# Performance work log

Measured on AMD Instinct MI355X. Metric: run time of the kernel, lower is better.

The kernel has to match this reference:

```python
import jax, jax.numpy as jnp
import numpy as np

B, T, I, H, O = 512, 1024, 15, 64, 11

def setup_inputs() -> dict:
    key = jax.random.key(0)
    ks = jax.random.split(key, 7)
    s_ih = 1.0 / np.sqrt(H)
    return {
        "x": jax.random.normal(ks[0], (B, T, I), dtype=jnp.float32),
        # torch nn.RNN params: weight_ih_l0 [H,I], weight_hh_l0 [H,H], biases [H]
        "W_ih": jax.random.uniform(ks[1], (H, I), jnp.float32, -s_ih, s_ih),
        "b_ih": jax.random.uniform(ks[2], (H,), jnp.float32, -s_ih, s_ih),
        "W_hh": jax.random.uniform(ks[3], (H, H), jnp.float32, -s_ih, s_ih),
        "b_hh": jax.random.uniform(ks[4], (H,), jnp.float32, -s_ih, s_ih),
        # decoder Linear(64, 11)
        "W_dec": jax.random.uniform(ks[5], (O, H), jnp.float32, -s_ih, s_ih),
        "b_dec": jax.random.uniform(ks[6], (O,), jnp.float32, -s_ih, s_ih),
    }

def reference(x, W_ih, b_ih, W_hh, b_hh, W_dec, b_dec):
    # Precompute input projection for all timesteps: [T, B, H]
    xproj = jnp.einsum("bti,hi->tbh", x, W_ih) + b_ih + b_hh
    h0 = jnp.zeros((x.shape[0], W_hh.shape[0]), dtype=x.dtype)

    def step(h, xp_t):
        h_new = jax.nn.relu(xp_t + h @ W_hh.T)  # [B, H]
        return h_new, h_new

    h_last, hs = jax.lax.scan(step, h0, xproj)  # hs: [T, B, H]
    out_seq = jnp.transpose(hs, (1, 0, 2))       # [B, T, H]
    out = jax.nn.relu(jnp.einsum("bth,oh->bto", out_seq, W_dec) + b_dec)
    h = h_last[None]  # [1, B, H] matching torch num_layers dim
    return (out, h)
```

## Files before the change

### kernel.cpp

```cpp
#include <hip/hip_runtime.h>
#include <hip/hip_fp16.h>
#include <stdint.h>

#define BB 512
#define TT 1024
#define II 15
#define HH 64
#define OO 11
#define NC (TT / 64)

typedef __fp16 half2v __attribute__((ext_vector_type(2)));
typedef _Float16 half8 __attribute__((ext_vector_type(8)));
typedef float floatx4 __attribute__((ext_vector_type(4)));
typedef int int4v __attribute__((ext_vector_type(4)));

union PK { int i; half2v h; float f; };
union AU { int4v i; half8 h; };

__device__ __forceinline__ half2v i2h2(int v) { PK u; u.i = v; return u.h; }
__device__ __forceinline__ int h22i(half2v v) { PK u; u.h = v; return u.i; }

__device__ __forceinline__ float FDOT2(half2v a, half2v b, float c) {
    return __builtin_amdgcn_fdot2(a, b, c, false);
}

__device__ __forceinline__ float lane_xor1(float v) {
    PK u; u.f = v;
    u.i = __builtin_amdgcn_mov_dpp(u.i, 0xB1, 0xF, 0xF, false);
    return u.f;
}

__device__ __forceinline__ float lane_xor2(float v) {
    PK u; u.f = v;
    u.i = __builtin_amdgcn_mov_dpp(u.i, 0x4E, 0xF, 0xF, false);
    return u.f;
}

__device__ __forceinline__ void block_sync() {
    asm volatile("s_waitcnt lgkmcnt(0)" ::: "memory");
    __builtin_amdgcn_s_barrier();
}

__global__ __launch_bounds__(256) void rnn_fused(
    const float* __restrict__ x, const float* __restrict__ W_ih,
    const float* __restrict__ b_ih, const float* __restrict__ W_hh,
    const float* __restrict__ b_hh, const float* __restrict__ W_dec,
    const float* __restrict__ b_dec, float* __restrict__ out,
    float* __restrict__ h_last)
{
    __shared__ __align__(16) int xpack[2][64 * 8];
    __shared__ __align__(16) float xsbuf[2][2][64 * 64];
    __shared__ __align__(16) _Float16 hring[2][128][HH];
    const int tid  = threadIdx.x;
    const int lane = tid & 63;
    const int wid  = tid >> 6;
    const int w = wid & 1;
    const int b = blockIdx.x * 2 + w;
    const float* xb = x + (size_t)b * TT * II;

    if (wid < 2) {
        const int nl = lane & 15;
        const int kq = lane >> 4;
        half8 bf[4][2];
#pragma unroll
        for (int g = 0; g < 4; ++g)
#pragma unroll
            for (int s = 0; s < 2; ++s)
#pragma unroll
                for (int j = 0; j < 8; ++j)
                    bf[g][s][j] = (_Float16)W_hh[(16 * g + nl) * HH +
                                                 32 * s + 8 * kq + j];

        int bpidx[8];
#pragma unroll
        for (int jj = 0; jj < 4; ++jj) {
            bpidx[jj]     = kq * 32 + 8 * jj;
            bpidx[jj + 4] = bpidx[jj] + 128;
        }
        const bool bsel4 = (lane & 16) != 0;
        const bool bsel5 = (lane & 32) != 0;
        const floatx4 zc = {0.0f, 0.0f, 0.0f, 0.0f};

        block_sync();

        float h = 0.0f;
        int hpk = 0;

        for (int c = 0; c < NC; ++c) {
            const float* xsp = &xsbuf[w][c & 1][0];
            for (int to = 0; to < 64; to += 8) {
#pragma unroll
                for (int u = 0; u < 8; ++u) {
                    const int ts = to + u;
                    const int t = c * 64 + ts;
                    const float xsv = xsp[ts * 64 + lane];

                    const int r0 = __builtin_amdgcn_ds_bpermute(bpidx[0], hpk);
                    const int r1 = __builtin_amdgcn_ds_bpermute(bpidx[1], hpk);
                    const int r2 = __builtin_amdgcn_ds_bpermute(bpidx[2], hpk);
                    const int r3 = __builtin_amdgcn_ds_bpermute(bpidx[3], hpk);
                    const int r4 = __builtin_amdgcn_ds_bpermute(bpidx[4], hpk);
                    const int r5 = __builtin_amdgcn_ds_bpermute(bpidx[5], hpk);
                    const int r6 = __builtin_amdgcn_ds_bpermute(bpidx[6], hpk);
                    const int r7 = __builtin_amdgcn_ds_bpermute(bpidx[7], hpk);
                    AU au0; au0.i = (int4v){r0, r1, r2, r3};
                    AU au1; au1.i = (int4v){r4, r5, r6, r7};
                    const half8 a0 = au0.h;
                    const half8 a1 = au1.h;

                    floatx4 c0 = __builtin_amdgcn_mfma_f32_16x16x32_f16(a0, bf[0][0], zc, 0, 0, 0);
                    floatx4 d0 = __builtin_amdgcn_mfma_f32_16x16x32_f16(a1, bf[0][1], zc, 0, 0, 0);
                    floatx4 c1 = __builtin_amdgcn_mfma_f32_16x16x32_f16(a0, bf[1][0], zc, 0, 0, 0);
                    floatx4 d1 = __builtin_amdgcn_mfma_f32_16x16x32_f16(a1, bf[1][1], zc, 0, 0, 0);
                    floatx4 c2 = __builtin_amdgcn_mfma_f32_16x16x32_f16(a0, bf[2][0], zc, 0, 0, 0);
                    floatx4 d2 = __builtin_amdgcn_mfma_f32_16x16x32_f16(a1, bf[2][1], zc, 0, 0, 0);
                    floatx4 c3 = __builtin_amdgcn_mfma_f32_16x16x32_f16(a0, bf[3][0], zc, 0, 0, 0);
                    floatx4 d3 = __builtin_amdgcn_mfma_f32_16x16x32_f16(a1, bf[3][1], zc, 0, 0, 0);

                    const float v0 = c0[0] + d0[0];
                    const float v1 = c1[0] + d1[0];
                    const float v2 = c2[0] + d2[0];
                    const float v3 = c3[0] + d3[0];
                    const float r01 = bsel4 ? v1 : v0;
                    const float r23 = bsel4 ? v3 : v2;
                    const float hpre = bsel5 ? r23 : r01;

                    h = fmaxf(hpre + xsv, 0.0f);
                    hring[w][t & 127][lane] = (_Float16)h;

                    hpk = h22i(__builtin_amdgcn_cvt_pkrtz(h, lane_xor1(h)));
                }
            }
            block_sync();
        }
        h_last[b * HH + lane] = h;
    } else {
        half2v wx[8];
#pragma unroll
        for (int j = 0; j < 7; ++j)
            wx[j] = __builtin_amdgcn_cvt_pkrtz(W_ih[lane * II + 2 * j],
                                               W_ih[lane * II + 2 * j + 1]);
        wx[7] = __builtin_amdgcn_cvt_pkrtz(W_ih[lane * II + 14],
                                           b_ih[lane] + b_hh[lane]);

        const int od = lane >> 2;
        const int oc = (od < OO) ? od : 0;
        const int ks = lane & 3;
        half2v wdec[8];
#pragma unroll
        for (int p = 0; p < 8; ++p)
            wdec[p] = __builtin_amdgcn_cvt_pkrtz(
                W_dec[oc * HH + (ks * 8 + p) * 2],
                W_dec[oc * HH + (ks * 8 + p) * 2 + 1]);
        const float bd = b_dec[oc];
        const bool dostore = (ks == 0) && (od < OO);
        float* outb = out + (size_t)b * TT * OO + od;

        auto stage_xs = [&](int chunk) __attribute__((always_inline)) {
            const float* xc = xb + (size_t)(chunk * 64 + lane) * II;
            float cf[II];
#pragma unroll
            for (int i = 0; i < II; ++i) cf[i] = xc[i];
            int4v p0, p1;
            p0.x = h22i(__builtin_amdgcn_cvt_pkrtz(cf[0], cf[1]));
            p0.y = h22i(__builtin_amdgcn_cvt_pkrtz(cf[2], cf[3]));
            p0.z = h22i(__builtin_amdgcn_cvt_pkrtz(cf[4], cf[5]));
            p0.w = h22i(__builtin_amdgcn_cvt_pkrtz(cf[6], cf[7]));
            p1.x = h22i(__builtin_amdgcn_cvt_pkrtz(cf[8], cf[9]));
            p1.y = h22i(__builtin_amdgcn_cvt_pkrtz(cf[10], cf[11]));
            p1.z = h22i(__builtin_amdgcn_cvt_pkrtz(cf[12], cf[13]));
            p1.w = h22i(__builtin_amdgcn_cvt_pkrtz(cf[14], 1.0f));
            *(int4v*)&xpack[w][lane * 8] = p0;
            *(int4v*)&xpack[w][lane * 8 + 4] = p1;

            const int4v* xp4 = (const int4v*)&xpack[w][0];
            float* xsd = &xsbuf[w][chunk & 1][0];
#pragma unroll 4
            for (int ts = 0; ts < 64; ++ts) {
                const int4v xv0 = xp4[2 * ts];
                const int4v xv1 = xp4[2 * ts + 1];
                float t0 = FDOT2(i2h2(xv0.x), wx[0], 0.0f);
                float t1 = FDOT2(i2h2(xv0.y), wx[1], 0.0f);
                float t2 = FDOT2(i2h2(xv0.z), wx[2], 0.0f);
                float t3 = FDOT2(i2h2(xv0.w), wx[3], 0.0f);
                float t4 = FDOT2(i2h2(xv1.x), wx[4], 0.0f);
                float t5 = FDOT2(i2h2(xv1.y), wx[5], 0.0f);
                float t6 = FDOT2(i2h2(xv1.z), wx[6], 0.0f);
                float t7 = FDOT2(i2h2(xv1.w), wx[7], 0.0f);
                xsd[ts * 64 + lane] = ((t0 + t1) + (t2 + t3)) +
                                      ((t4 + t5) + (t6 + t7));
            }
        };

        auto decode_chunk = [&](int c) __attribute__((always_inline)) {
#pragma unroll 4
            for (int lt = 0; lt < 64; ++lt) {
                const int t = c * 64 + lt;
                const char* row = (const char*)&hring[w][t & 127][0];
                const int4v d0 = *(const int4v*)(row + ks * 32);
                const int4v d1 = *(const int4v*)(row + ks * 32 + 16);
                float dacc = FDOT2(i2h2(d0.x), wdec[0], 0.0f);
                dacc = FDOT2(i2h2(d0.y), wdec[1], dacc);
                dacc = FDOT2(i2h2(d0.z), wdec[2], dacc);
                dacc = FDOT2(i2h2(d0.w), wdec[3], dacc);
                dacc = FDOT2(i2h2(d1.x), wdec[4], dacc);
                dacc = FDOT2(i2h2(d1.y), wdec[5], dacc);
                dacc = FDOT2(i2h2(d1.z), wdec[6], dacc);
                dacc = FDOT2(i2h2(d1.w), wdec[7], dacc);
                dacc += lane_xor1(dacc);
                dacc += lane_xor2(dacc);
                if (dostore)
                    outb[(size_t)t * OO] = fmaxf(dacc + bd, 0.0f);
            }
        };

        stage_xs(0);
        block_sync();

        for (int c = 0; c < NC; ++c) {
            if (c + 1 < NC) stage_xs(c + 1);
            if (c >= 1) decode_chunk(c - 1);
            block_sync();
        }
        decode_chunk(NC - 1);
    }
}

extern "C" void kernel_launch(void* const* d_in, const int* in_sizes, int n_in,
                              void* d_out, int out_size, void* d_ws, size_t ws_size,
                              hipStream_t stream) {
    const float* x     = (const float*)d_in[0];
    const float* W_ih  = (const float*)d_in[1];
    const float* b_ih  = (const float*)d_in[2];
    const float* W_hh  = (const float*)d_in[3];
    const float* b_hh  = (const float*)d_in[4];
    const float* W_dec = (const float*)d_in[5];
    const float* b_dec = (const float*)d_in[6];

    float* out    = (float*)d_out;
    float* h_last = out + (size_t)BB * TT * OO;

    rnn_fused<<<BB / 2, 256, 0, stream>>>(x, W_ih, b_ih, W_hh, b_hh,
                                          W_dec, b_dec, out, h_last);
}
```

Baseline: 251.3 us.

## Interleave two batch recurrences in one wave and halve block size

Each block now uses one recurrence wave that advances two independent batch rows in lockstep, issuing both rows' bpermutes before their MFMAs. A single helper wave stages the input projections and decodes outputs for both rows. The aim is to hide the latency of the serial per-step dependency chain by overlapping two chains in one wave, instead of using two mostly stalled waves. The risk is that the single helper wave, now doing double the work per chunk, becomes the bottleneck, and that the longer per-step instruction stream lengthens the critical path.

```diff
diff --git a/kernel.cpp b/kernel.cpp
--- a/kernel.cpp
+++ b/kernel.cpp
@@ -41,24 +41,23 @@
     __builtin_amdgcn_s_barrier();
 }
 
-__global__ __launch_bounds__(256) void rnn_fused(
+__global__ __launch_bounds__(128) void rnn_fused(
     const float* __restrict__ x, const float* __restrict__ W_ih,
     const float* __restrict__ b_ih, const float* __restrict__ W_hh,
     const float* __restrict__ b_hh, const float* __restrict__ W_dec,
     const float* __restrict__ b_dec, float* __restrict__ out,
     float* __restrict__ h_last)
 {
-    __shared__ __align__(16) int xpack[2][64 * 8];
+    __shared__ __align__(16) int xpack[64 * 8];
     __shared__ __align__(16) float xsbuf[2][2][64 * 64];
     __shared__ __align__(16) _Float16 hring[2][128][HH];
     const int tid  = threadIdx.x;
     const int lane = tid & 63;
     const int wid  = tid >> 6;
-    const int w = wid & 1;
-    const int b = blockIdx.x * 2 + w;
-    const float* xb = x + (size_t)b * TT * II;
-
-    if (wid < 2) {
+    const int bA = blockIdx.x * 2;
+    const int bB = bA + 1;
+
+    if (wid == 0) {
         const int nl = lane & 15;
         const int kq = lane >> 4;
         half8 bf[4][2];
@@ -83,57 +82,79 @@
 
         block_sync();
 
-        float h = 0.0f;
-        int hpk = 0;
+        float hA = 0.0f, hB = 0.0f;
+        int hpkA = 0, hpkB = 0;
 
         for (int c = 0; c < NC; ++c) {
-            const float* xsp = &xsbuf[w][c & 1][0];
+            const float* xspA = &xsbuf[0][c & 1][0];
+            const float* xspB = &xsbuf[1][c & 1][0];
             for (int to = 0; to < 64; to += 8) {
 #pragma unroll
                 for (int u = 0; u < 8; ++u) {
                     const int ts = to + u;
                     const int t = c * 64 + ts;
-                    const float xsv = xsp[ts * 64 + lane];
-
-                    const int r0 = __builtin_amdgcn_ds_bpermute(bpidx[0], hpk);
-                    const int r1 = __builtin_amdgcn_ds_bpermute(bpidx[1], hpk);
-                    const int r2 = __builtin_amdgcn_ds_bpermute(bpidx[2], hpk);
-                    const int r3 = __builtin_amdgcn_ds_bpermute(bpidx[3], hpk);
-                    const int r4 = __builtin_amdgcn_ds_bpermute(bpidx[4], hpk);
-                    const int r5 = __builtin_amdgcn_ds_bpermute(bpidx[5], hpk);
-                    const int r6 = __builtin_amdgcn_ds_bpermute(bpidx[6], hpk);
-                    const int r7 = __builtin_amdgcn_ds_bpermute(bpidx[7], hpk);
-                    AU au0; au0.i = (int4v){r0, r1, r2, r3};
-                    AU au1; au1.i = (int4v){r4, r5, r6, r7};
-                    const half8 a0 = au0.h;
-                    const half8 a1 = au1.h;
-
-                    floatx4 c0 = __builtin_amdgcn_mfma_f32_16x16x32_f16(a0, bf[0][0], zc, 0, 0, 0);
-                    floatx4 d0 = __builtin_amdgcn_mfma_f32_16x16x32_f16(a1, bf[0][1], zc, 0, 0, 0);
-                    floatx4 c1 = __builtin_amdgcn_mfma_f32_16x16x32_f16(a0, bf[1][0], zc, 0, 0, 0);
-                    floatx4 d1 = __builtin_amdgcn_mfma_f32_16x16x32_f16(a1, bf[1][1], zc, 0, 0, 0);
-                    floatx4 c2 = __builtin_amdgcn_mfma_f32_16x16x32_f16(a0, bf[2][0], zc, 0, 0, 0);
-                    floatx4 d2 = __builtin_amdgcn_mfma_f32_16x16x32_f16(a1, bf[2][1], zc, 0, 0, 0);
-                    floatx4 c3 = __builtin_amdgcn_mfma_f32_16x16x32_f16(a0, bf[3][0], zc, 0, 0, 0);
-                    floatx4 d3 = __builtin_amdgcn_mfma_f32_16x16x32_f16(a1, bf[3][1], zc, 0, 0, 0);
-
-                    const float v0 = c0[0] + d0[0];
-                    const float v1 = c1[0] + d1[0];
-                    const float v2 = c2[0] + d2[0];
-                    const float v3 = c3[0] + d3[0];
-                    const float r01 = bsel4 ? v1 : v0;
-                    const float r23 = bsel4 ? v3 : v2;
-                    const float hpre = bsel5 ? r23 : r01;
-
-                    h = fmaxf(hpre + xsv, 0.0f);
-                    hring[w][t & 127][lane] = (_Float16)h;
-
-                    hpk = h22i(__builtin_amdgcn_cvt_pkrtz(h, lane_xor1(h)));
+                    const float xsvA = xspA[ts * 64 + lane];
+                    const float xsvB = xspB[ts * 64 + lane];
+
+                    int rA[8], rB[8];
+#pragma unroll
+                    for (int j = 0; j < 8; ++j)
+                        rA[j] = __builtin_amdgcn_ds_bpermute(bpidx[j], hpkA);
+#pragma unroll
+                    for (int j = 0; j < 8; ++j)
+                        rB[j] = __builtin_amdgcn_ds_bpermute(bpidx[j], hpkB);
+                    __builtin_amdgcn_sched_barrier(0);
+
+                    {
+                        AU u0; u0.i = (int4v){rA[0], rA[1], rA[2], rA[3]};
+                        AU u1; u1.i = (int4v){rA[4], rA[5], rA[6], rA[7]};
+                        const half8 a0 = u0.h, a1 = u1.h;
+                        floatx4 c0 = __builtin_amdgcn_mfma_f32_16x16x32_f16(a0, bf[0][0], zc, 0, 0, 0);
+                        floatx4 d0 = __builtin_amdgcn_mfma_f32_16x16x32_f16(a1, bf[0][1], zc, 0, 0, 0);
+                        floatx4 c1 = __builtin_amdgcn_mfma_f32_16x16x32_f16(a0, bf[1][0], zc, 0, 0, 0);
+                        floatx4 d1 = __builtin_amdgcn_mfma_f32_16x16x32_f16(a1, bf[1][1], zc, 0, 0, 0);
+                        floatx4 c2 = __builtin_amdgcn_mfma_f32_16x16x32_f16(a0, bf[2][0], zc, 0, 0, 0);
+                        floatx4 d2 = __builtin_amdgcn_mfma_f32_16x16x32_f16(a1, bf[2][1], zc, 0, 0, 0);
+                        floatx4 c3 = __builtin_amdgcn_mfma_f32_16x16x32_f16(a0, bf[3][0], zc, 0, 0, 0);
+                        floatx4 d3 = __builtin_amdgcn_mfma_f32_16x16x32_f16(a1, bf[3][1], zc, 0, 0, 0);
+                        const float v0 = c0[0] + d0[0];
+                        const float v1 = c1[0] + d1[0];
+                        const float v2 = c2[0] + d2[0];
+                        const float v3 = c3[0] + d3[0];
+                        const float r01 = bsel4 ? v1 : v0;
+                        const float r23 = bsel4 ? v3 : v2;
+                        hA = fmaxf((bsel5 ? r23 : r01) + xsvA, 0.0f);
+                        hring[0][t & 127][lane] = (_Float16)hA;
+                        hpkA = h22i(__builtin_amdgcn_cvt_pkrtz(hA, lane_xor1(hA)));
+                    }
+                    {
+                        AU u0; u0.i = (int4v){rB[0], rB[1], rB[2], rB[3]};
+                        AU u1; u1.i = (int4v){rB[4], rB[5], rB[6], rB[7]};
+                        const half8 a0 = u0.h, a1 = u1.h;
+                        floatx4 c0 = __builtin_amdgcn_mfma_f32_16x16x32_f16(a0, bf[0][0], zc, 0, 0, 0);
+                        floatx4 d0 = __builtin_amdgcn_mfma_f32_16x16x32_f16(a1, bf[0][1], zc, 0, 0, 0);
+                        floatx4 c1 = __builtin_amdgcn_mfma_f32_16x16x32_f16(a0, bf[1][0], zc, 0, 0, 0);
+                        floatx4 d1 = __builtin_amdgcn_mfma_f32_16x16x32_f16(a1, bf[1][1], zc, 0, 0, 0);
+                        floatx4 c2 = __builtin_amdgcn_mfma_f32_16x16x32_f16(a0, bf[2][0], zc, 0, 0, 0);
+                        floatx4 d2 = __builtin_amdgcn_mfma_f32_16x16x32_f16(a1, bf[2][1], zc, 0, 0, 0);
+                        floatx4 c3 = __builtin_amdgcn_mfma_f32_16x16x32_f16(a0, bf[3][0], zc, 0, 0, 0);
+                        floatx4 d3 = __builtin_amdgcn_mfma_f32_16x16x32_f16(a1, bf[3][1], zc, 0, 0, 0);
+                        const float v0 = c0[0] + d0[0];
+                        const float v1 = c1[0] + d1[0];
+                        const float v2 = c2[0] + d2[0];
+                        const float v3 = c3[0] + d3[0];
+                        const float r01 = bsel4 ? v1 : v0;
+                        const float r23 = bsel4 ? v3 : v2;
+                        hB = fmaxf((bsel5 ? r23 : r01) + xsvB, 0.0f);
+                        hring[1][t & 127][lane] = (_Float16)hB;
+                        hpkB = h22i(__builtin_amdgcn_cvt_pkrtz(hB, lane_xor1(hB)));
+                    }
                 }
             }
             block_sync();
         }
-        h_last[b * HH + lane] = h;
+        h_last[bA * HH + lane] = hA;
+        h_last[bB * HH + lane] = hB;
     } else {
         half2v wx[8];
 #pragma unroll
@@ -154,10 +175,14 @@
                 W_dec[oc * HH + (ks * 8 + p) * 2 + 1]);
         const float bd = b_dec[oc];
         const bool dostore = (ks == 0) && (od < OO);
-        float* outb = out + (size_t)b * TT * OO + od;
-
-        auto stage_xs = [&](int chunk) __attribute__((always_inline)) {
-            const float* xc = xb + (size_t)(chunk * 64 + lane) * II;
+
+        const float* xbc[2] = { x + (size_t)bA * TT * II,
+                                x + (size_t)bB * TT * II };
+        float* outc[2] = { out + (size_t)bA * TT * OO + od,
+                           out + (size_t)bB * TT * OO + od };
+
+        auto stage_xs = [&](int ch, int chunk) __attribute__((always_inline)) {
+            const float* xc = xbc[ch] + (size_t)(chunk * 64 + lane) * II;
             float cf[II];
 #pragma unroll
             for (int i = 0; i < II; ++i) cf[i] = xc[i];
@@ -170,11 +195,11 @@
             p1.y = h22i(__builtin_amdgcn_cvt_pkrtz(cf[10], cf[11]));
             p1.z = h22i(__builtin_amdgcn_cvt_pkrtz(cf[12], cf[13]));
             p1.w = h22i(__builtin_amdgcn_cvt_pkrtz(cf[14], 1.0f));
-            *(int4v*)&xpack[w][lane * 8] = p0;
-            *(int4v*)&xpack[w][lane * 8 + 4] = p1;
-
-            const int4v* xp4 = (const int4v*)&xpack[w][0];
-            float* xsd = &xsbuf[w][chunk & 1][0];
+            *(int4v*)&xpack[lane * 8] = p0;
+            *(int4v*)&xpack[lane * 8 + 4] = p1;
+
+            const int4v* xp4 = (const int4v*)&xpack[0];
+            float* xsd = &xsbuf[ch][chunk & 1][0];
 #pragma unroll 4
             for (int ts = 0; ts < 64; ++ts) {
                 const int4v xv0 = xp4[2 * ts];
@@ -192,11 +217,11 @@
             }
         };
 
-        auto decode_chunk = [&](int c) __attribute__((always_inline)) {
+        auto decode_chunk = [&](int ch, int c) __attribute__((always_inline)) {
 #pragma unroll 4
             for (int lt = 0; lt < 64; ++lt) {
                 const int t = c * 64 + lt;
-                const char* row = (const char*)&hring[w][t & 127][0];
+                const char* row = (const char*)&hring[ch][t & 127][0];
                 const int4v d0 = *(const int4v*)(row + ks * 32);
                 const int4v d1 = *(const int4v*)(row + ks * 32 + 16);
                 float dacc = FDOT2(i2h2(d0.x), wdec[0], 0.0f);
@@ -210,19 +235,21 @@
                 dacc += lane_xor1(dacc);
                 dacc += lane_xor2(dacc);
                 if (dostore)
-                    outb[(size_t)t * OO] = fmaxf(dacc + bd, 0.0f);
+                    outc[ch][(size_t)t * OO] = fmaxf(dacc + bd, 0.0f);
             }
         };
 
-        stage_xs(0);
+        stage_xs(0, 0);
+        stage_xs(1, 0);
         block_sync();
 
         for (int c = 0; c < NC; ++c) {
-            if (c + 1 < NC) stage_xs(c + 1);
-            if (c >= 1) decode_chunk(c - 1);
+            if (c + 1 < NC) { stage_xs(0, c + 1); stage_xs(1, c + 1); }
+            if (c >= 1)     { decode_chunk(0, c - 1); decode_chunk(1, c - 1); }
             block_sync();
         }
-        decode_chunk(NC - 1);
+        decode_chunk(0, NC - 1);
+        decode_chunk(1, NC - 1);
     }
 }
 
@@ -240,6 +267,6 @@
     float* out    = (float*)d_out;
     float* h_last = out + (size_t)BB * TT * OO;
 
-    rnn_fused<<<BB / 2, 256, 0, stream>>>(x, W_ih, b_ih, W_hh, b_hh,
+    rnn_fused<<<BB / 2, 128, 0, stream>>>(x, W_ih, b_ih, W_hh, b_hh,
                                           W_dec, b_dec, out, h_last);
 }
```

Measured after the change: 412.1 us. 1.64x slower.
